# Kernel optimization log

Hardware: AMD Instinct MI355X
Metric: run time of the kernel (lower is better)

## Reference

```python
import jax, jax.numpy as jnp
import numpy as np

Q_HEADS, KV_HEADS, DIMS, IN_DIMS = 16, 4, 1024, 1024
HEAD_D = DIMS // Q_HEADS            # 64
GROUPS = Q_HEADS // KV_HEADS        # 4
ROPE_BASE = 10000.0


def nd_rope(x, coords):
    """N-D rotary embedding.
    x: [..., s, d]; coords: broadcastable [..., s, a] (float).
    Head dim d is split into a contiguous chunks of d//a; within each chunk
    consecutive pairs (2i, 2i+1) are rotated by angle coord_axis * base^(-2i/(d//a)).
    """
    a = coords.shape[-1]
    d = x.shape[-1]
    dpa = d // a                                  # dims per coordinate axis (even)
    inv_freq = ROPE_BASE ** (-jnp.arange(dpa // 2, dtype=jnp.float32) * (2.0 / dpa))
    angles = coords[..., :, None] * inv_freq      # [..., s, a, dpa//2]
    angles = angles.reshape(angles.shape[:-2] + (d // 2,))
    cos, sin = jnp.cos(angles), jnp.sin(angles)
    xp = x.reshape(x.shape[:-1] + (d // 2, 2))
    x1, x2 = xp[..., 0], xp[..., 1]
    return jnp.stack([x1 * cos - x2 * sin, x1 * sin + x2 * cos], axis=-1).reshape(x.shape)


def setup_inputs() -> dict:
    key = jax.random.key(0)
    k1, k2, k3, k4, k5, k6, k7, k8 = jax.random.split(key, 8)
    B, SQ, SKV, A = 4, 2048, 2048, 2
    q = jax.random.normal(k1, (B, SQ, IN_DIMS), dtype=jnp.float32)
    kv = jax.random.normal(k2, (B, SKV, IN_DIMS), dtype=jnp.float32)
    q_coords = jax.random.randint(k3, (B, SQ, A), 0, 2048, dtype=jnp.int32)
    kv_coords = jax.random.randint(k4, (B, SKV, A), 0, 2048, dtype=jnp.int32)
    s_in = 1.0 / np.sqrt(IN_DIMS)
    Wq = jax.random.normal(k5, (IN_DIMS, Q_HEADS, HEAD_D), dtype=jnp.float32) * s_in
    Wk = jax.random.normal(k6, (IN_DIMS, KV_HEADS, HEAD_D), dtype=jnp.float32) * s_in
    Wv = jax.random.normal(k7, (IN_DIMS, KV_HEADS, HEAD_D), dtype=jnp.float32) * s_in
    Wo = jax.random.normal(k8, (KV_HEADS * HEAD_D, IN_DIMS), dtype=jnp.float32) * (1.0 / np.sqrt(KV_HEADS * HEAD_D))
    return {"q": q, "q_coords": q_coords, "kv": kv, "kv_coords": kv_coords,
            "Wq": Wq, "Wk": Wk, "Wv": Wv, "Wo": Wo}


def reference(q, q_coords, kv, kv_coords, Wq, Wk, Wv, Wo):
    B, SQ = q.shape[0], q.shape[1]
    qp = jnp.einsum('bsi,ihd->bshd', q, Wq)   # [b, sq, q_heads, hd]
    kp = jnp.einsum('bsi,ihd->bshd', kv, Wk)  # [b, skv, kv_heads, hd]
    vp = jnp.einsum('bsi,ihd->bshd', kv, Wv)
    # '... s (h g) d -> ... g h s d' with h=KV_HEADS outer, g=GROUPS inner
    qp = qp.reshape(B, SQ, KV_HEADS, GROUPS, HEAD_D).transpose(0, 3, 2, 1, 4)  # [b,g,h,sq,hd]
    kp = kp.transpose(0, 2, 1, 3)  # [b,h,skv,hd]
    vp = vp.transpose(0, 2, 1, 3)
    qc = q_coords.astype(jnp.float32)[:, None, None]  # [b,1,1,sq,a] -> broadcast over g,h
    kc = kv_coords.astype(jnp.float32)[:, None]       # [b,1,skv,a] -> broadcast over h
    qr = nd_rope(qp, qc)
    kr = nd_rope(kp, kc)
    # NOTE: einops pattern omits g in output -> group axis is SUMMED (faithful to source)
    scores = jnp.einsum('bghsd,bhad->bhsa', qr, kr) / (HEAD_D ** 0.5)
    attn = jax.nn.softmax(scores, axis=-1)
    out = jnp.einsum('bhsa,bhad->bhsd', attn, vp)
    out = out.transpose(0, 2, 1, 3).reshape(B, SQ, KV_HEADS * HEAD_D)
    return out @ Wo
```

## Files before the change

### kernel.cpp

```cpp
#include <hip/hip_runtime.h>

#define BATCH 4
#define SEQQ  2048
#define SEQKV 2048
#define NH    4
#define HD    64
#define IND   1024
#define QSCL 0.18033688011112042f

typedef __attribute__((ext_vector_type(8))) short short8;
typedef __attribute__((ext_vector_type(4))) short s4v;
typedef __attribute__((ext_vector_type(4))) float floatx4;

#if defined(__HIP_DEVICE_COMPILE__) && __has_builtin(__builtin_amdgcn_exp2f)
  #define EXP2(x) __builtin_amdgcn_exp2f(x)
#else
  #define EXP2(x) exp2f(x)
#endif

#if defined(__HIP_DEVICE_COMPILE__)
  #if __has_builtin(__builtin_amdgcn_mfma_f32_16x16x16bf16_1k)
    #define MFMA16(a, b, c) __builtin_amdgcn_mfma_f32_16x16x16bf16_1k(a, b, c, 0, 0, 0)
  #elif __has_builtin(__builtin_amdgcn_mfma_f32_16x16x16_bf16)
    #define MFMA16(a, b, c) __builtin_amdgcn_mfma_f32_16x16x16_bf16(a, b, c, 0, 0, 0)
  #else
    #error "no 16x16x16 bf16 MFMA builtin on gfx950 device pass"
  #endif
#else
  #define MFMA16(a, b, c) (c)
#endif
#define MFMA32(a, b, c) __builtin_amdgcn_mfma_f32_16x16x32_bf16(a, b, c, 0, 0, 0)

__device__ __forceinline__ short f2b(float f) {
    unsigned u; __builtin_memcpy(&u, &f, 4);
    u = (u + 0x7fffu + ((u >> 16) & 1u)) >> 16;
    return (short)u;
}
__device__ __forceinline__ short8 cvt8(const float* p) {
    float4 a = *(const float4*)p;
    float4 b = *(const float4*)(p + 4);
    short8 r;
    r[0] = f2b(a.x); r[1] = f2b(a.y); r[2] = f2b(a.z); r[3] = f2b(a.w);
    r[4] = f2b(b.x); r[5] = f2b(b.y); r[6] = f2b(b.z); r[7] = f2b(b.w);
    return r;
}

__global__ __launch_bounds__(256) void prep_all(
    const float* __restrict__ Wq, const float* __restrict__ Wk,
    const float* __restrict__ Wv, const float* __restrict__ Wo,
    const float* __restrict__ q, const float* __restrict__ kv,
    short* __restrict__ Wq_t, short* __restrict__ Wkv_t, short* __restrict__ Wo_t,
    short* __restrict__ qb, short* __restrict__ kvb) {
    __shared__ short Ts[64][65];
    int blk = blockIdx.x;
    if (blk < 256) {
        int c4 = threadIdx.x & 63, r4 = threadIdx.x >> 6;
        if (blk < 64) {
            int h = blk & 3, ib = blk >> 2;
#pragma unroll 4
            for (int jj = 0; jj < 16; ++jj) {
                int il = r4 * 16 + jj;
                float s = 0.f;
#pragma unroll
                for (int g = 0; g < 4; ++g)
                    s += Wq[(ib * 64 + il) * 1024 + (h * 4 + g) * 64 + c4];
                Ts[il][c4] = f2b(s);
            }
            __syncthreads();
#pragma unroll 4
            for (int jj = 0; jj < 16; ++jj) {
                int dl = r4 * 16 + jj;
                Wq_t[(h * 64 + dl) * 1024 + ib * 64 + c4] = Ts[c4][dl];
            }
        } else if (blk < 192) {
            int t = blk - 64, ss = t >> 6; t &= 63;
            int ib = t >> 2, nb = t & 3;
            const float* W = ss ? Wv : Wk;
#pragma unroll 4
            for (int jj = 0; jj < 16; ++jj) {
                int il = r4 * 16 + jj;
                Ts[il][c4] = f2b(W[(ib * 64 + il) * 256 + nb * 64 + c4]);
            }
            __syncthreads();
#pragma unroll 4
            for (int jj = 0; jj < 16; ++jj) {
                int dl = r4 * 16 + jj;
                Wkv_t[(ss * 256 + nb * 64 + dl) * 1024 + ib * 64 + c4] = Ts[c4][dl];
            }
        } else {
            int t = blk - 192, kb = t >> 4, nb = t & 15;
#pragma unroll 4
            for (int jj = 0; jj < 16; ++jj) {
                int il = r4 * 16 + jj;
                Ts[il][c4] = f2b(Wo[(kb * 64 + il) * 1024 + nb * 64 + c4]);
            }
            __syncthreads();
#pragma unroll 4
            for (int jj = 0; jj < 16; ++jj) {
                int dl = r4 * 16 + jj;
                Wo_t[(nb * 64 + dl) * 256 + kb * 64 + c4] = Ts[c4][dl];
            }
        }
    } else if (blk < 2304) {
        long e = ((long)(blk - 256) * 256 + threadIdx.x) * 16;
        *(short8*)(qb + e)     = cvt8(q + e);
        *(short8*)(qb + e + 8) = cvt8(q + e + 8);
    } else {
        long e = ((long)(blk - 2304) * 256 + threadIdx.x) * 16;
        *(short8*)(kvb + e)     = cvt8(kv + e);
        *(short8*)(kvb + e + 8) = cvt8(kv + e + 8);
    }
}

template <int MODE>
__device__ __forceinline__ void gemm128(
    const short* __restrict__ A, const short* __restrict__ Wt,
    int m0, int n0, int N, int K, short* As, short* Bs,
    float* __restrict__ C, const int* __restrict__ coords,
    short* __restrict__ ropeDst, short* __restrict__ vDst) {
    const int t = threadIdx.x;
    const int w = t >> 6, lane = t & 63, ln = lane & 15, quad = lane >> 4;
    const int wm = w >> 1, wn = w & 1;
    const int srow = lane >> 2, skc = (lane & 3) * 8;
    floatx4 acc[4][4];
#pragma unroll
    for (int mt = 0; mt < 4; ++mt)
#pragma unroll
        for (int nt = 0; nt < 4; ++nt) acc[mt][nt] = floatx4{0.f, 0.f, 0.f, 0.f};

    auto stage = [&](int ks, int sel) {
#pragma unroll
        for (int i = 0; i < 2; ++i) {
            __builtin_amdgcn_global_load_lds(
                (const void*)(A + (long)(m0 + w * 32 + i * 16 + srow) * K + ks + skc),
                (void*)(As + sel * 4096 + (w * 2 + i) * 512), 16, 0, 0);
            __builtin_amdgcn_global_load_lds(
                (const void*)(Wt + (long)(n0 + w * 32 + i * 16 + srow) * K + ks + skc),
                (void*)(Bs + sel * 4096 + (w * 2 + i) * 512), 16, 0, 0);
        }
    };

    const int nk = K >> 5;
    stage(0, 0);
    __syncthreads();
    int cur = 0;
    for (int tt = 0; tt < nk; ++tt) {
        if (tt < nk - 1) stage((tt + 1) * 32, cur ^ 1);
        const short* Ac = As + cur * 4096;
        const short* Bc = Bs + cur * 4096;
        short8 af[4], bf[4];
#pragma unroll
        for (int mt = 0; mt < 4; ++mt)
            af[mt] = *(const short8*)(Ac + (wm * 64 + mt * 16 + ln) * 32 + quad * 8);
#pragma unroll
        for (int nt = 0; nt < 4; ++nt)
            bf[nt] = *(const short8*)(Bc + (wn * 64 + nt * 16 + ln) * 32 + quad * 8);
#pragma unroll
        for (int mt = 0; mt < 4; ++mt)
#pragma unroll
            for (int nt = 0; nt < 4; ++nt)
                acc[mt][nt] = MFMA32(af[mt], bf[nt], acc[mt][nt]);
        __syncthreads();
        cur ^= 1;
    }

    if (MODE == 0) {
#pragma unroll
        for (int mt = 0; mt < 4; ++mt) {
            int row0 = m0 + wm * 64 + mt * 16 + quad * 4;
#pragma unroll
            for (int nt = 0; nt < 4; ++nt) {
                int col = n0 + wn * 64 + nt * 16 + ln;
#pragma unroll
                for (int r = 0; r < 4; ++r)
                    C[(long)(row0 + r) * N + col] = acc[mt][nt][r];
            }
        }
    } else {
        const int wn_col = n0 + wn * 64;
        if (MODE == 1 || wn_col < 256) {
            const int h = (wn_col >> 6) & 3;
            const float scl = (MODE == 1) ? QSCL : 1.0f;
            const float L = -0.5756462732485114f;
            const float fA = __expf((float)(ln >> 1) * L);
            const float fB = __expf((float)(8 + (ln >> 1)) * L);
            const float sgn = (ln & 1) ? 1.0f : -1.0f;
#pragma unroll
            for (int mt = 0; mt < 4; ++mt) {
                int row0 = m0 + wm * 64 + mt * 16 + quad * 4;
#pragma unroll
                for (int r = 0; r < 4; ++r) {
                    int row = row0 + r;
                    float c0 = (float)coords[row * 2];
                    float c1 = (float)coords[row * 2 + 1];
                    float snv[4], csv[4];
                    __sincosf(c0 * fA, &snv[0], &csv[0]);
                    __sincosf(c0 * fB, &snv[1], &csv[1]);
                    __sincosf(c1 * fA, &snv[2], &csv[2]);
                    __sincosf(c1 * fB, &snv[3], &csv[3]);
                    long rbase = ((long)((row >> 11) * 4 + h) * 2048 + (row & 2047)) * 64;
#pragma unroll
                    for (int nt = 0; nt < 4; ++nt) {
                        float v = acc[mt][nt][r];
                        float p = __shfl_xor(v, 1, 64);
                        float o = v * (csv[nt] * scl) + p * (snv[nt] * (scl * sgn));
                        ropeDst[rbase + nt * 16 + ln] = f2b(o);
                    }
                }
            }
        } else {
            const int h = ((wn_col - 256) >> 6) & 3;
#pragma unroll
            for (int mt = 0; mt < 4; ++mt) {
                int row0 = m0 + wm * 64 + mt * 16 + quad * 4;
                int b = row0 >> 11, s0 = row0 & 2047;
#pragma unroll
                for (int nt = 0; nt < 4; ++nt) {
                    s4v ov;
#pragma unroll
                    for (int r = 0; r < 4; ++r) ov[r] = f2b(acc[mt][nt][r]);
                    *(s4v*)(vDst + (long)((b * 4 + h) * 64 + nt * 16 + ln) * 2048 + s0) = ov;
                }
            }
        }
    }
}

__global__ __launch_bounds__(256) void proj_gemm(
    const short* __restrict__ qb, const short* __restrict__ kvb,
    const short* __restrict__ Wq_t, const short* __restrict__ Wkv_t,
    const int* __restrict__ qc, const int* __restrict__ kvc,
    short* __restrict__ Qr, short* __restrict__ Kr, short* __restrict__ Vt) {
    __shared__ __align__(16) short As[2][128 * 32];
    __shared__ __align__(16) short Bs[2][128 * 32];
    int id = blockIdx.x;
    if (id < 128)
        gemm128<1>(qb, Wq_t, (id >> 1) * 128, (id & 1) * 128, 256, 1024,
                   &As[0][0], &Bs[0][0], nullptr, qc, Qr, nullptr);
    else {
        int t = id - 128;
        gemm128<2>(kvb, Wkv_t, (t >> 2) * 128, (t & 3) * 128, 512, 1024,
                   &As[0][0], &Bs[0][0], nullptr, kvc, Kr, Vt);
    }
}

__global__ __launch_bounds__(256) void final_gemm(
    const short* __restrict__ Ob, const short* __restrict__ Wo_t, float* __restrict__ out) {
    __shared__ __align__(16) short As[2][128 * 32];
    __shared__ __align__(16) short Bs[2][128 * 32];
    gemm128<0>(Ob, Wo_t, blockIdx.x * 128, blockIdx.y * 128, 1024, 256,
               &As[0][0], &Bs[0][0], out, nullptr, nullptr, nullptr);
}

__global__ __launch_bounds__(256, 4) void attn_kernel(
    const short* __restrict__ Qr, const short* __restrict__ Kr,
    const short* __restrict__ Vt, short* __restrict__ Ob) {
    __shared__ __align__(16) short Kls[2][64 * 64];
    __shared__ __align__(16) short Vls[2][64 * 64];
    const int blk = blockIdx.x;
    const int x = blk & 7, y = blk >> 3;
    const int bh = x * 2 + (y >> 5), qg = y & 31;
    const int w = threadIdx.x >> 6, lane = threadIdx.x & 63;
    const int ln = lane & 15, quad = lane >> 4;
    const int q0 = qg * 64 + w * 16;
    const short* Qb = Qr + (long)bh * SEQKV * HD;
    const short* Kb = Kr + (long)bh * SEQKV * HD;
    const short* Vb = Vt + (long)bh * HD * SEQKV;

    const int srow = lane >> 3;
    const int schk = (lane & 7) ^ (srow & 7);
    const long kstage0 = (long)(w * 16 + srow) * HD + schk * 8;
    const long vstage0 = (long)(w * 16 + srow) * SEQKV + schk * 8;

    short8 qf[2];
#pragma unroll
    for (int ck = 0; ck < 2; ++ck)
        qf[ck] = *(const short8*)(Qb + (long)(q0 + ln) * HD + ck * 32 + quad * 8);

    s4v ones;
#pragma unroll
    for (int j = 0; j < 4; ++j) ones[j] = (short)0x3F80;

    floatx4 o[4], ol;
    ol = floatx4{0.f, 0.f, 0.f, 0.f};
#pragma unroll
    for (int nt = 0; nt < 4; ++nt) o[nt] = floatx4{0.f, 0.f, 0.f, 0.f};

    const int ln7 = ln & 7;
    int koff[2];
#pragma unroll
    for (int ck = 0; ck < 2; ++ck) koff[ck] = ln * 64 + ((ck * 4 + quad) ^ ln7) * 8;
    int voff[4];
#pragma unroll
    for (int t = 0; t < 4; ++t) voff[t] = ln * 64 + ((t * 2 + (quad >> 1)) ^ ln7) * 8 + (quad & 1) * 4;

#define STAGE(kt, sel)                                                              \
    do {                                                                            \
        _Pragma("unroll")                                                           \
        for (int i = 0; i < 2; ++i) {                                               \
            __builtin_amdgcn_global_load_lds(                                       \
                (const void*)(Kb + (long)(kt) * HD + kstage0 + (long)i * 8 * HD),   \
                (void*)(&Kls[sel][(w * 16 + i * 8) * 64]), 16, 0, 0);               \
            __builtin_amdgcn_global_load_lds(                                       \
                (const void*)(Vb + (kt) + vstage0 + (long)i * 8 * SEQKV),           \
                (void*)(&Vls[sel][(w * 16 + i * 8) * 64]), 16, 0, 0);               \
        }                                                                           \
    } while (0)

    STAGE(0, 0);
    __syncthreads();
    int cur = 0;
    for (int tt = 0; tt < 32; ++tt) {
        if (tt < 31) STAGE((tt + 1) * 64, cur ^ 1);
        const short* Kc = &Kls[cur][0];
        const short* Vc = &Vls[cur][0];
#pragma unroll
        for (int t = 0; t < 4; ++t) {
            short8 a0 = *(const short8*)(Kc + t * 1024 + koff[0]);
            short8 a1 = *(const short8*)(Kc + t * 1024 + koff[1]);
            floatx4 st = {0.f, 0.f, 0.f, 0.f};
            __builtin_amdgcn_s_setprio(1);
            st = MFMA32(a0, qf[0], st);
            st = MFMA32(a1, qf[1], st);
            __builtin_amdgcn_s_setprio(0);
            float e0 = EXP2(st[0]), e1 = EXP2(st[1]), e2 = EXP2(st[2]), e3 = EXP2(st[3]);
            unsigned p0, p1;
            asm("v_cvt_pk_bf16_f32 %0, %1, %2" : "=v"(p0) : "v"(e0), "v"(e1));
            asm("v_cvt_pk_bf16_f32 %0, %1, %2" : "=v"(p1) : "v"(e2), "v"(e3));
            s4v pt;
            { unsigned tmp[2] = {p0, p1}; __builtin_memcpy(&pt, tmp, 8); }
            __builtin_amdgcn_s_setprio(1);
#pragma unroll
            for (int nt = 0; nt < 4; ++nt) {
                s4v vf = *(const s4v*)(Vc + nt * 1024 + voff[t]);
                o[nt] = MFMA16(vf, pt, o[nt]);
            }
            ol = MFMA16(ones, pt, ol);
            __builtin_amdgcn_s_setprio(0);
        }
        __syncthreads();
        cur ^= 1;
    }
#undef STAGE
    const int b = bh >> 2, h = bh & 3;
    const float li = 1.0f / ol[0];
    const long base = ((long)(b * 2048 + q0 + ln)) * 256 + h * 64;
#pragma unroll
    for (int nt = 0; nt < 4; ++nt) {
        s4v ov;
#pragma unroll
        for (int r = 0; r < 4; ++r) ov[r] = f2b(o[nt][r] * li);
        *(s4v*)(Ob + base + nt * 16 + quad * 4) = ov;
    }
}

extern "C" void kernel_launch(void* const* d_in, const int* in_sizes, int n_in,
                              void* d_out, int out_size, void* d_ws, size_t ws_size,
                              hipStream_t stream) {
    const float* q   = (const float*)d_in[0];
    const int*   qc  = (const int*)d_in[1];
    const float* kv  = (const float*)d_in[2];
    const int*   kvc = (const int*)d_in[3];
    const float* Wq  = (const float*)d_in[4];
    const float* Wk  = (const float*)d_in[5];
    const float* Wv  = (const float*)d_in[6];
    const float* Wo  = (const float*)d_in[7];
    float* out = (float*)d_out;

    char* ws = (char*)d_ws;
    const size_t MB = 1024 * 1024;
    short* Wq_t  = (short*)(ws);
    short* Wkv_t = (short*)(ws + MB / 2);
    short* Wo_t  = (short*)(ws + 3 * MB / 2);
    short* qb    = (short*)(ws + 2 * MB);
    short* kvb   = (short*)(ws + 18 * MB);
    short* Qr    = (short*)(ws + 34 * MB);
    short* Kr    = (short*)(ws + 38 * MB);
    short* Vt    = (short*)(ws + 42 * MB);
    short* Ob    = (short*)(ws + 46 * MB);

    hipLaunchKernelGGL(prep_all, dim3(4352), dim3(256), 0, stream,
                       Wq, Wk, Wv, Wo, q, kv, Wq_t, Wkv_t, Wo_t, qb, kvb);
    hipLaunchKernelGGL(proj_gemm, dim3(384), dim3(256), 0, stream,
                       qb, kvb, Wq_t, Wkv_t, qc, kvc, Qr, Kr, Vt);
    hipLaunchKernelGGL(attn_kernel, dim3(512), dim3(256), 0, stream,
                       Qr, Kr, Vt, Ob);
    hipLaunchKernelGGL(final_gemm, dim3(64, 8), dim3(256), 0, stream, Ob, Wo_t, out);
}
```

Measured before the change: 203.0 us.

## Split attention KV sequence across two wave groups and reduce partials in LDS

```diff
diff --git a/kernel.cpp b/kernel.cpp
--- a/kernel.cpp
+++ b/kernel.cpp
@@ -252,25 +252,26 @@
                &As[0][0], &Bs[0][0], out, nullptr, nullptr, nullptr);
 }
 
-__global__ __launch_bounds__(256, 4) void attn_kernel(
+__global__ __launch_bounds__(512, 4) void attn_kernel(
     const short* __restrict__ Qr, const short* __restrict__ Kr,
     const short* __restrict__ Vt, short* __restrict__ Ob) {
-    __shared__ __align__(16) short Kls[2][64 * 64];
-    __shared__ __align__(16) short Vls[2][64 * 64];
+    __shared__ __align__(16) short Kls[2][2][64 * 64];
+    __shared__ __align__(16) short Vls[2][2][64 * 64];
     const int blk = blockIdx.x;
     const int x = blk & 7, y = blk >> 3;
     const int bh = x * 2 + (y >> 5), qg = y & 31;
     const int w = threadIdx.x >> 6, lane = threadIdx.x & 63;
+    const int qw = w & 3, half = w >> 2;
     const int ln = lane & 15, quad = lane >> 4;
-    const int q0 = qg * 64 + w * 16;
+    const int q0 = qg * 64 + qw * 16;
     const short* Qb = Qr + (long)bh * SEQKV * HD;
-    const short* Kb = Kr + (long)bh * SEQKV * HD;
-    const short* Vb = Vt + (long)bh * HD * SEQKV;
+    const short* Kb = Kr + (long)bh * SEQKV * HD + (long)half * 1024 * HD;
+    const short* Vb = Vt + (long)bh * HD * SEQKV + half * 1024;
 
     const int srow = lane >> 3;
     const int schk = (lane & 7) ^ (srow & 7);
-    const long kstage0 = (long)(w * 16 + srow) * HD + schk * 8;
-    const long vstage0 = (long)(w * 16 + srow) * SEQKV + schk * 8;
+    const long kstage0 = (long)(qw * 16 + srow) * HD + schk * 8;
+    const long vstage0 = (long)(qw * 16 + srow) * SEQKV + schk * 8;
 
     short8 qf[2];
 #pragma unroll
@@ -294,26 +295,26 @@
 #pragma unroll
     for (int t = 0; t < 4; ++t) voff[t] = ln * 64 + ((t * 2 + (quad >> 1)) ^ ln7) * 8 + (quad & 1) * 4;
 
-#define STAGE(kt, sel)                                                              \
-    do {                                                                            \
-        _Pragma("unroll")                                                           \
-        for (int i = 0; i < 2; ++i) {                                               \
-            __builtin_amdgcn_global_load_lds(                                       \
-                (const void*)(Kb + (long)(kt) * HD + kstage0 + (long)i * 8 * HD),   \
-                (void*)(&Kls[sel][(w * 16 + i * 8) * 64]), 16, 0, 0);               \
-            __builtin_amdgcn_global_load_lds(                                       \
-                (const void*)(Vb + (kt) + vstage0 + (long)i * 8 * SEQKV),           \
-                (void*)(&Vls[sel][(w * 16 + i * 8) * 64]), 16, 0, 0);               \
-        }                                                                           \
+#define STAGE(kt, sel)                                                                \
+    do {                                                                              \
+        _Pragma("unroll")                                                             \
+        for (int i = 0; i < 2; ++i) {                                                 \
+            __builtin_amdgcn_global_load_lds(                                         \
+                (const void*)(Kb + (long)(kt) * HD + kstage0 + (long)i * 8 * HD),     \
+                (void*)(&Kls[half][sel][(qw * 16 + i * 8) * 64]), 16, 0, 0);          \
+            __builtin_amdgcn_global_load_lds(                                         \
+                (const void*)(Vb + (kt) + vstage0 + (long)i * 8 * SEQKV),             \
+                (void*)(&Vls[half][sel][(qw * 16 + i * 8) * 64]), 16, 0, 0);          \
+        }                                                                             \
     } while (0)
 
     STAGE(0, 0);
     __syncthreads();
     int cur = 0;
-    for (int tt = 0; tt < 32; ++tt) {
-        if (tt < 31) STAGE((tt + 1) * 64, cur ^ 1);
-        const short* Kc = &Kls[cur][0];
-        const short* Vc = &Vls[cur][0];
+    for (int tt = 0; tt < 16; ++tt) {
+        if (tt < 15) STAGE((tt + 1) * 64, cur ^ 1);
+        const short* Kc = &Kls[half][cur][0];
+        const short* Vc = &Vls[half][cur][0];
 #pragma unroll
         for (int t = 0; t < 4; ++t) {
             short8 a0 = *(const short8*)(Kc + t * 1024 + koff[0]);
@@ -342,15 +343,27 @@
         cur ^= 1;
     }
 #undef STAGE
-    const int b = bh >> 2, h = bh & 3;
-    const float li = 1.0f / ol[0];
-    const long base = ((long)(b * 2048 + q0 + ln)) * 256 + h * 64;
-#pragma unroll
-    for (int nt = 0; nt < 4; ++nt) {
-        s4v ov;
-#pragma unroll
-        for (int r = 0; r < 4; ++r) ov[r] = f2b(o[nt][r] * li);
-        *(s4v*)(Ob + base + nt * 16 + quad * 4) = ov;
+    float* cb = (float*)&Kls[0][0][0];
+    const int slot = (qw * 64 + lane) * 20;
+    if (half == 1) {
+#pragma unroll
+        for (int nt = 0; nt < 4; ++nt)
+            *(floatx4*)(cb + slot + nt * 4) = o[nt];
+        cb[slot + 16] = ol[0];
+    }
+    __syncthreads();
+    if (half == 0) {
+        const int b = bh >> 2, h = bh & 3;
+        const float li = 1.0f / (ol[0] + cb[slot + 16]);
+        const long base = ((long)(b * 2048 + q0 + ln)) * 256 + h * 64;
+#pragma unroll
+        for (int nt = 0; nt < 4; ++nt) {
+            floatx4 o2 = *(const floatx4*)(cb + slot + nt * 4);
+            s4v ov;
+#pragma unroll
+            for (int r = 0; r < 4; ++r) ov[r] = f2b((o[nt][r] + o2[r]) * li);
+            *(s4v*)(Ob + base + nt * 16 + quad * 4) = ov;
+        }
     }
 }
 
@@ -383,7 +396,7 @@
                        Wq, Wk, Wv, Wo, q, kv, Wq_t, Wkv_t, Wo_t, qb, kvb);
     hipLaunchKernelGGL(proj_gemm, dim3(384), dim3(256), 0, stream,
                        qb, kvb, Wq_t, Wkv_t, qc, kvc, Qr, Kr, Vt);
-    hipLaunchKernelGGL(attn_kernel, dim3(512), dim3(256), 0, stream,
+    hipLaunchKernelGGL(attn_kernel, dim3(512), dim3(512), 0, stream,
                        Qr, Kr, Vt, Ob);
     hipLaunchKernelGGL(final_gemm, dim3(64, 8), dim3(256), 0, stream, Ob, Wo_t, out);
 }
```

New measurement: 190.1 us. -6.4%, faster.
